# Kernel tuning notes

Hardware: AMD Instinct MI355X
Metric: run time of the kernel (lower is better)

## Reference

```python
import jax, jax.numpy as jnp
import numpy as np
import math

TWO_PI = 2.0 * math.pi

OUT_C = 384
IN_C = 384
K = 16          # group_kernel_size (grid_H.shape[0])
NUM_IN = 16     # num_in_H
NUM_OUT = 16    # num_out_H


def setup_inputs() -> dict:
    key = jax.random.key(0)
    k1, k2, k3 = jax.random.split(key, 3)
    in_H = jax.random.uniform(k1, (NUM_IN, 1), dtype=jnp.float32) * TWO_PI
    out_H = jax.random.uniform(k2, (NUM_OUT, 1), dtype=jnp.float32) * TWO_PI
    # kaiming_uniform-like init for weight [out, in//groups, K]
    fan_in = IN_C * K
    bound = math.sqrt(6.0 / ((1 + 5.0) * fan_in))
    weight = jax.random.uniform(k3, (OUT_C, IN_C, K), dtype=jnp.float32,
                                minval=-bound, maxval=bound)
    # uniform SO(2) grid of angles, shape [K, 1]
    grid_H = (jnp.arange(K, dtype=jnp.float32) * (TWO_PI / K))[:, None]
    return {"in_H": in_H, "out_H": out_H, "weight": weight, "grid_H": grid_H}


def reference(in_H, out_H, weight, grid_H):
    num_in, num_out = in_H.shape[0], out_H.shape[0]
    k = grid_H.shape[0]
    out_c, in_c, _ = weight.shape

    # inverse_H on SO(2): negate angle
    out_H_inv = -out_H                                   # [num_out, 1]
    # left_apply_to_H(out_H_inv, in_H): group composition, broadcast so the
    # flattened result views as (num_in, num_out, ...)
    prod = jnp.mod(in_H[:, None, :] + out_H_inv[None, :, :], TWO_PI)  # [num_in, num_out, 1]
    coords = prod.reshape(-1)                             # [S], S = num_in*num_out

    # signal on group grid: weight.transpose(0,2).reshape(K, -1)
    signal = jnp.transpose(weight, (2, 1, 0)).reshape(k, -1)  # [K, in_c*out_c]

    # interpolate_H: circular linear interpolation on uniform angle grid
    spacing = TWO_PI / k
    pos = coords / spacing                                # [S]
    base = jnp.floor(pos)
    i0 = jnp.mod(base.astype(jnp.int32), k)
    i1 = jnp.mod(i0 + 1, k)
    frac = (pos - base)[:, None]                          # [S, 1]
    interp = (1.0 - frac) * signal[i0] + frac * signal[i1]  # [S, in_c*out_c]

    # view(num_in, num_out, in_c, out_c, 1, 1).transpose(0,3).transpose(1,3)
    w = interp.reshape(num_in, num_out, in_c, out_c, 1, 1)
    w = jnp.transpose(w, (3, 1, 2, 0, 4, 5))  # swap axes 0,3
    w = jnp.transpose(w, (0, 3, 2, 1, 4, 5))  # swap axes 1,3
    return w  # [out_c, num_in, in_c, num_out, 1, 1]
```

## Files before the change

kernel.cpp:

```cpp
#include <hip/hip_runtime.h>
#include <math.h>

#define OUT_C   384
#define IN_C    384
#define KG      16
#define NUM_IN  16
#define NUM_OUT 16
#define ICH     192
#define PAD     17

__global__ __launch_bounds__(256) void gsub_kernel(
    const float* __restrict__ in_H,
    const float* __restrict__ out_H,
    const float* __restrict__ weight,
    float* __restrict__ out)
{
    __shared__ float s_frac[NUM_IN * NUM_OUT];
    __shared__ int   s_i0[NUM_IN * NUM_OUT];
    __shared__ float s_w[ICH * PAD];

    const int t  = threadIdx.x;
    const int b  = blockIdx.x;
    const int oc = b >> 2;
    const int h  = (b >> 1) & 1;
    const int nh = b & 1;
    const int ic_base = h * ICH;

    {
        const int ni = t >> 4;
        const int no = t & 15;
        const float TWOPI = 6.283185307179586f;
        float c = in_H[ni] - out_H[no];
        float r = fmodf(c, TWOPI);
        if (r < 0.0f) r += TWOPI;
        float pos = r * ((float)KG / TWOPI);
        float bse = floorf(pos);
        s_i0[t]   = ((int)bse) & (KG - 1);
        s_frac[t] = pos - bse;
    }

    const float4* wsrc = (const float4*)(weight + ((size_t)oc * IN_C + ic_base) * KG);
    #pragma unroll
    for (int j = 0; j < 3; ++j) {
        int f = t + j * 256;
        float4 v = wsrc[f];
        int ic_l = f >> 2;
        int kq   = (f & 3) * 4;
        float* dst = &s_w[ic_l * PAD + kq];
        dst[0] = v.x; dst[1] = v.y; dst[2] = v.z; dst[3] = v.w;
        if ((f & 3) == 0) s_w[ic_l * PAD + 16] = v.x;
    }
    __syncthreads();

    const int q   = t & 3;
    const int lic = t >> 2;

    float4* op = (float4*)out + (size_t)oc * 24576 + (size_t)(ic_base + lic) * 4 + q;
    const int fb = 4 * q;
    const int ni0 = nh * 8;

    for (int ni = ni0; ni < ni0 + 8; ++ni) {
        const float* fr = &s_frac[ni * 16 + fb];
        const int*   iz = &s_i0[ni * 16 + fb];
        float f0 = fr[0], f1 = fr[1], f2 = fr[2], f3 = fr[3];
        int   a0 = iz[0], a1 = iz[1], a2 = iz[2], a3 = iz[3];

        #pragma unroll
        for (int r = 0; r < 3; ++r) {
            const float* wrow = &s_w[(r * 64 + lic) * PAD];
            float x0 = wrow[a0], y0 = wrow[a0 + 1];
            float x1 = wrow[a1], y1 = wrow[a1 + 1];
            float x2 = wrow[a2], y2 = wrow[a2 + 1];
            float x3 = wrow[a3], y3 = wrow[a3 + 1];
            float4 v;
            v.x = fmaf(f0, y0 - x0, x0);
            v.y = fmaf(f1, y1 - x1, x1);
            v.z = fmaf(f2, y2 - x2, x2);
            v.w = fmaf(f3, y3 - x3, x3);
            op[ni * 1536 + r * 256] = v;
        }
    }
}

extern "C" void kernel_launch(void* const* d_in, const int* in_sizes, int n_in,
                              void* d_out, int out_size, void* d_ws, size_t ws_size,
                              hipStream_t stream) {
    const float* in_H   = (const float*)d_in[0];
    const float* out_H  = (const float*)d_in[1];
    const float* weight = (const float*)d_in[2];
    float* o = (float*)d_out;
    gsub_kernel<<<OUT_C * 4, 256, 0, stream>>>(in_H, out_H, weight, o);
}
```

Baseline: 30.67 us.

## Use persistent 512-thread blocks looping over three weight units each

The kernel now launches 256 blocks of 512 threads. Each block loops over three (oc, half) units and computes the interpolation table only once per block. Each unit writes its 16 full ni rows, where before two separate blocks each handled 8 rows and both reloaded the same weight slice. This removes the duplicated weight loads and table setup and keeps the stores contiguous. In exchange it uses fewer blocks (256 on a large GPU), adds barriers per unit, and adds integer division in the address computation.

```diff
diff --git a/kernel.cpp b/kernel.cpp
--- a/kernel.cpp
+++ b/kernel.cpp
@@ -8,8 +8,9 @@
 #define NUM_OUT 16
 #define ICH     192
 #define PAD     17
+#define UPB     3
 
-__global__ __launch_bounds__(256) void gsub_kernel(
+__global__ __launch_bounds__(512) void gsub_kernel(
     const float* __restrict__ in_H,
     const float* __restrict__ out_H,
     const float* __restrict__ weight,
@@ -19,14 +20,9 @@
     __shared__ int   s_i0[NUM_IN * NUM_OUT];
     __shared__ float s_w[ICH * PAD];
 
-    const int t  = threadIdx.x;
-    const int b  = blockIdx.x;
-    const int oc = b >> 2;
-    const int h  = (b >> 1) & 1;
-    const int nh = b & 1;
-    const int ic_base = h * ICH;
+    const int t = threadIdx.x;
 
-    {
+    if (t < 256) {
         const int ni = t >> 4;
         const int no = t & 15;
         const float TWOPI = 6.283185307179586f;
@@ -39,45 +35,54 @@
         s_frac[t] = pos - bse;
     }
 
-    const float4* wsrc = (const float4*)(weight + ((size_t)oc * IN_C + ic_base) * KG);
-    #pragma unroll
-    for (int j = 0; j < 3; ++j) {
-        int f = t + j * 256;
-        float4 v = wsrc[f];
-        int ic_l = f >> 2;
-        int kq   = (f & 3) * 4;
-        float* dst = &s_w[ic_l * PAD + kq];
-        dst[0] = v.x; dst[1] = v.y; dst[2] = v.z; dst[3] = v.w;
-        if ((f & 3) == 0) s_w[ic_l * PAD + 16] = v.x;
-    }
-    __syncthreads();
+    for (int u0 = 0; u0 < UPB; ++u0) {
+        const int unit = blockIdx.x * UPB + u0;
+        const int oc = unit >> 1;
+        const int h  = unit & 1;
 
-    const int q   = t & 3;
-    const int lic = t >> 2;
+        __syncthreads();
 
-    float4* op = (float4*)out + (size_t)oc * 24576 + (size_t)(ic_base + lic) * 4 + q;
-    const int fb = 4 * q;
-    const int ni0 = nh * 8;
+        const float4* wsrc = (const float4*)(weight + ((size_t)oc * IN_C + h * ICH) * KG);
+        {
+            float4 v = wsrc[t];
+            int ic_l = t >> 2, kq = (t & 3) * 4;
+            float* dst = &s_w[ic_l * PAD + kq];
+            dst[0] = v.x; dst[1] = v.y; dst[2] = v.z; dst[3] = v.w;
+            if ((t & 3) == 0) s_w[ic_l * PAD + 16] = v.x;
+        }
+        if (t < 256) {
+            int f = 512 + t;
+            float4 v = wsrc[f];
+            int ic_l = f >> 2, kq = (f & 3) * 4;
+            float* dst = &s_w[ic_l * PAD + kq];
+            dst[0] = v.x; dst[1] = v.y; dst[2] = v.z; dst[3] = v.w;
+            if ((f & 3) == 0) s_w[ic_l * PAD + 16] = v.x;
+        }
+        __syncthreads();
 
-    for (int ni = ni0; ni < ni0 + 8; ++ni) {
-        const float* fr = &s_frac[ni * 16 + fb];
-        const int*   iz = &s_i0[ni * 16 + fb];
-        float f0 = fr[0], f1 = fr[1], f2 = fr[2], f3 = fr[3];
-        int   a0 = iz[0], a1 = iz[1], a2 = iz[2], a3 = iz[3];
+        float4* ob = (float4*)out + (size_t)oc * 24576 + (size_t)h * 768;
+        #pragma unroll
+        for (int i = 0; i < 24; ++i) {
+            int f  = i * 512 + t;
+            int ni = f / 768;
+            int g  = f - ni * 768;
+            int lic = g >> 2;
+            int qb  = (g & 3) * 4;
 
-        #pragma unroll
-        for (int r = 0; r < 3; ++r) {
-            const float* wrow = &s_w[(r * 64 + lic) * PAD];
-            float x0 = wrow[a0], y0 = wrow[a0 + 1];
-            float x1 = wrow[a1], y1 = wrow[a1 + 1];
-            float x2 = wrow[a2], y2 = wrow[a2 + 1];
-            float x3 = wrow[a3], y3 = wrow[a3 + 1];
+            const float* wrow = &s_w[lic * PAD];
+            const float* fr   = &s_frac[ni * 16 + qb];
+            const int*   iz   = &s_i0[ni * 16 + qb];
+
+            float x0 = wrow[iz[0]], y0 = wrow[iz[0] + 1];
+            float x1 = wrow[iz[1]], y1 = wrow[iz[1] + 1];
+            float x2 = wrow[iz[2]], y2 = wrow[iz[2] + 1];
+            float x3 = wrow[iz[3]], y3 = wrow[iz[3] + 1];
             float4 v;
-            v.x = fmaf(f0, y0 - x0, x0);
-            v.y = fmaf(f1, y1 - x1, x1);
-            v.z = fmaf(f2, y2 - x2, x2);
-            v.w = fmaf(f3, y3 - x3, x3);
-            op[ni * 1536 + r * 256] = v;
+            v.x = fmaf(fr[0], y0 - x0, x0);
+            v.y = fmaf(fr[1], y1 - x1, x1);
+            v.z = fmaf(fr[2], y2 - x2, x2);
+            v.w = fmaf(fr[3], y3 - x3, x3);
+            ob[ni * 1536 + g] = v;
         }
     }
 }
@@ -89,5 +94,5 @@
     const float* out_H  = (const float*)d_in[1];
     const float* weight = (const float*)d_in[2];
     float* o = (float*)d_out;
-    gsub_kernel<<<OUT_C * 4, 256, 0, stream>>>(in_H, out_H, weight, o);
+    gsub_kernel<<<256, 512, 0, stream>>>(in_H, out_H, weight, o);
 }
```

After: 30.15 us. About the same (-1.7%).

## Give each block a full input-channel row and remap threads to wave-per-ni

Applied to the files above, without the earlier changes.

Each block now loads all 384 input channels of one output channel into shared memory, halving the grid to 768 blocks. Work is remapped so each wave handles two ni values and walks 24 channel groups, writing 64 contiguous float4 per wave per step. Weight loads are issued up front, before the coordinate setup, so their latency overlaps that computation. The block now holds twice the shared memory and the grid has fewer blocks, which may lower occupancy and parallelism.

```diff
diff --git a/kernel.cpp b/kernel.cpp
--- a/kernel.cpp
+++ b/kernel.cpp
@@ -6,7 +6,6 @@
 #define KG      16
 #define NUM_IN  16
 #define NUM_OUT 16
-#define ICH     192
 #define PAD     17
 
 __global__ __launch_bounds__(256) void gsub_kernel(
@@ -17,14 +16,20 @@
 {
     __shared__ float s_frac[NUM_IN * NUM_OUT];
     __shared__ int   s_i0[NUM_IN * NUM_OUT];
-    __shared__ float s_w[ICH * PAD];
+    __shared__ float s_w[IN_C * PAD];
 
     const int t  = threadIdx.x;
     const int b  = blockIdx.x;
-    const int oc = b >> 2;
-    const int h  = (b >> 1) & 1;
+    const int oc = b >> 1;
     const int nh = b & 1;
-    const int ic_base = h * ICH;
+
+    const float4* wsrc = (const float4*)(weight + (size_t)oc * IN_C * KG);
+    float4 v0 = wsrc[t];
+    float4 v1 = wsrc[t + 256];
+    float4 v2 = wsrc[t + 512];
+    float4 v3 = wsrc[t + 768];
+    float4 v4 = wsrc[t + 1024];
+    float4 v5 = wsrc[t + 1280];
 
     {
         const int ni = t >> 4;
@@ -39,45 +44,50 @@
         s_frac[t] = pos - bse;
     }
 
-    const float4* wsrc = (const float4*)(weight + ((size_t)oc * IN_C + ic_base) * KG);
-    #pragma unroll
-    for (int j = 0; j < 3; ++j) {
-        int f = t + j * 256;
-        float4 v = wsrc[f];
-        int ic_l = f >> 2;
-        int kq   = (f & 3) * 4;
-        float* dst = &s_w[ic_l * PAD + kq];
-        dst[0] = v.x; dst[1] = v.y; dst[2] = v.z; dst[3] = v.w;
-        if ((f & 3) == 0) s_w[ic_l * PAD + 16] = v.x;
+    {
+        float4 vv[6] = {v0, v1, v2, v3, v4, v5};
+        #pragma unroll
+        for (int k = 0; k < 6; ++k) {
+            int f = t + k * 256;
+            int ic_l = f >> 2;
+            int kq   = (f & 3) * 4;
+            float* dst = &s_w[ic_l * PAD + kq];
+            dst[0] = vv[k].x; dst[1] = vv[k].y; dst[2] = vv[k].z; dst[3] = vv[k].w;
+            if ((f & 3) == 0) s_w[ic_l * PAD + 16] = vv[k].x;
+        }
     }
     __syncthreads();
 
-    const int q   = t & 3;
-    const int lic = t >> 2;
+    const int w   = t >> 6;
+    const int L   = t & 63;
+    const int q   = L & 3;
+    const int icl = L >> 2;
+    const int fb  = 4 * q;
 
-    float4* op = (float4*)out + (size_t)oc * 24576 + (size_t)(ic_base + lic) * 4 + q;
-    const int fb = 4 * q;
-    const int ni0 = nh * 8;
+    float4* ob = (float4*)out + (size_t)oc * 24576;
 
-    for (int ni = ni0; ni < ni0 + 8; ++ni) {
+    #pragma unroll
+    for (int p = 0; p < 2; ++p) {
+        const int ni = nh * 8 + w * 2 + p;
         const float* fr = &s_frac[ni * 16 + fb];
         const int*   iz = &s_i0[ni * 16 + fb];
         float f0 = fr[0], f1 = fr[1], f2 = fr[2], f3 = fr[3];
         int   a0 = iz[0], a1 = iz[1], a2 = iz[2], a3 = iz[3];
 
-        #pragma unroll
-        for (int r = 0; r < 3; ++r) {
-            const float* wrow = &s_w[(r * 64 + lic) * PAD];
+        float4* run = ob + (size_t)ni * 1536 + L;
+        #pragma unroll 4
+        for (int j = 0; j < 24; ++j) {
+            const float* wrow = &s_w[(j * 16 + icl) * PAD];
             float x0 = wrow[a0], y0 = wrow[a0 + 1];
             float x1 = wrow[a1], y1 = wrow[a1 + 1];
             float x2 = wrow[a2], y2 = wrow[a2 + 1];
             float x3 = wrow[a3], y3 = wrow[a3 + 1];
-            float4 v;
-            v.x = fmaf(f0, y0 - x0, x0);
-            v.y = fmaf(f1, y1 - x1, x1);
-            v.z = fmaf(f2, y2 - x2, x2);
-            v.w = fmaf(f3, y3 - x3, x3);
-            op[ni * 1536 + r * 256] = v;
+            float4 vv;
+            vv.x = fmaf(f0, y0 - x0, x0);
+            vv.y = fmaf(f1, y1 - x1, x1);
+            vv.z = fmaf(f2, y2 - x2, x2);
+            vv.w = fmaf(f3, y3 - x3, x3);
+            run[j * 64] = vv;
         }
     }
 }
@@ -89,5 +99,5 @@
     const float* out_H  = (const float*)d_in[1];
     const float* weight = (const float*)d_in[2];
     float* o = (float*)d_out;
-    gsub_kernel<<<OUT_C * 4, 256, 0, stream>>>(in_H, out_H, weight, o);
+    gsub_kernel<<<OUT_C * 2, 256, 0, stream>>>(in_H, out_H, weight, o);
 }
```

After: 31.02 us. No clear change (+1.2%).
